# Kernel tuning notes

Hardware: AMD Instinct MI355X
Metric: run time of the kernel (lower is better)

Reference implementation:

```python
import jax, jax.numpy as jnp
import numpy as np

B, T, CIN = 8, 1024, 6
D, L = 128, 2
DI, DS, DC, DTR = 256, 32, 4, 8  # d_inner=expand*d_model, d_state, d_conv, dt_rank=ceil(D/16)
BN_EPS = 1e-5


def setup_inputs() -> dict:
    key = jax.random.key(0)
    ks = jax.random.split(key, 8)
    s = 0.02
    A_log = jnp.log(jnp.broadcast_to(jnp.arange(1, DS + 1, dtype=jnp.float32), (L, DI, DS)))  # S4D-real init
    return {
        "x": jax.random.normal(ks[0], (B, T, CIN), jnp.float32),
        "conv_fw": jax.random.normal(ks[1], (D, CIN, 3), jnp.float32) * s,
        "conv_fb": jnp.zeros((D,), jnp.float32),
        "bn_g": jnp.ones((D,), jnp.float32),
        "bn_b": jnp.zeros((D,), jnp.float32),
        "rms_w": jnp.ones((L, D), jnp.float32),
        "W_in": jax.random.normal(ks[2], (L, D, 2 * DI), jnp.float32) * s,
        "conv_w": jax.random.normal(ks[3], (L, DI, DC), jnp.float32) * s,
        "conv_b": jnp.zeros((L, DI), jnp.float32),
        "W_xproj": jax.random.normal(ks[4], (L, DI, DTR + 2 * DS), jnp.float32) * s,
        "W_dt": jax.random.normal(ks[5], (L, DTR, DI), jnp.float32) * s,
        "b_dt": jnp.zeros((L, DI), jnp.float32),
        "A_log": A_log,
        "D_param": jnp.ones((L, DI), jnp.float32),
        "W_out": jax.random.normal(ks[6], (L, DI, D), jnp.float32) * s,
        "alpha": jnp.full((L,), 0.6, jnp.float32),
        "beta": jnp.full((L,), 0.99, jnp.float32),
        "norm_w": jnp.ones((D,), jnp.float32),
    }


def rmsnorm(x, w, eps=1e-6):
    return x * w * jax.lax.rsqrt(jnp.mean(x * x, axis=-1, keepdims=True) + eps)


def _mamba_block(x, rms_w, W_in, conv_w, conv_b, W_xproj, W_dt, b_dt, A_log, D_param, W_out, a, b):
    # pre-norm residual momentum-Mamba block; x: (B,T,D)
    xz = rmsnorm(x, rms_w) @ W_in            # (B,T,2*DI)
    xc, z = jnp.split(xz, 2, axis=-1)
    # depthwise causal conv over time
    xc = jnp.transpose(xc, (0, 2, 1))        # (B,DI,T)
    xc = jax.lax.conv_general_dilated(xc, conv_w[:, None, :], (1,), [(DC - 1, 0)],
                                      dimension_numbers=("NCH", "OIH", "NCH"), feature_group_count=DI)
    xc = jax.nn.silu(xc + conv_b[None, :, None])
    xc = jnp.transpose(xc, (0, 2, 1))        # (B,T,DI)
    xdbl = xc @ W_xproj                      # (B,T,DTR+2*DS)
    dtl, Bm, Cm = jnp.split(xdbl, [DTR, DTR + DS], axis=-1)
    dt = jax.nn.softplus(dtl @ W_dt + b_dt)  # (B,T,DI)
    A = -jnp.exp(A_log)                      # (DI,DS)
    dA = jnp.exp(dt[..., None] * A)          # (B,T,DI,DS)
    dBx = (dt * xc)[..., None] * Bm[:, :, None, :]  # (B,T,DI,DS)

    def step(carry, inp):
        h, v = carry
        dA_t, dBx_t, C_t = inp
        v = b * v + dBx_t                    # momentum accumulator (mode='real')
        h = dA_t * h + (1.0 - a) * dBx_t + a * v
        y = jnp.einsum("bds,bs->bd", h, C_t)
        return (h, v), y

    h0 = jnp.zeros((x.shape[0], DI, DS), x.dtype)
    _, ys = jax.lax.scan(step, (h0, h0),
                         (jnp.swapaxes(dA, 0, 1), jnp.swapaxes(dBx, 0, 1), jnp.swapaxes(Cm, 0, 1)))
    y = jnp.swapaxes(ys, 0, 1) + D_param * xc
    y = y * jax.nn.silu(z)
    return x + y @ W_out


def reference(x, conv_fw, conv_fb, bn_g, bn_b, rms_w, W_in, conv_w, conv_b, W_xproj,
              W_dt, b_dt, A_log, D_param, W_out, alpha, beta, norm_w):
    # frontend: Conv1d(k=3,pad=1) + BatchNorm1d(eval, running mean 0 var 1) + ReLU (dropout=identity in eval)
    h = jax.lax.conv_general_dilated(jnp.transpose(x, (0, 2, 1)), conv_fw, (1,), [(1, 1)],
                                     dimension_numbers=("NCH", "OIH", "NCH"))
    h = h + conv_fb[None, :, None]
    h = h * (bn_g / jnp.sqrt(1.0 + BN_EPS))[None, :, None] + bn_b[None, :, None]
    h = jax.nn.relu(h)
    h = jnp.transpose(h, (0, 2, 1))          # (B,T,D)
    for i in range(L):
        h = _mamba_block(h, rms_w[i], W_in[i], conv_w[i], conv_b[i], W_xproj[i], W_dt[i],
                         b_dt[i], A_log[i], D_param[i], W_out[i], alpha[i], beta[i])
    return rmsnorm(h, norm_w)
```

## Files before the change

kernel.cpp:

```cpp
#include <hip/hip_runtime.h>
#include <hip/hip_bf16.h>
#include <math.h>

constexpr int Bb  = 8;
constexpr int Tt  = 1024;
constexpr int CIN = 6;
constexpr int Dd  = 128;
constexpr int Ll  = 2;
constexpr int DI  = 256;
constexpr int DS  = 32;
constexpr int DC  = 4;
constexpr int DTR = 8;
constexpr int NX  = DTR + 2 * DS;
constexpr int NXP = 128;
constexpr int ROWS = Bb * Tt;

using u16 = unsigned short;
using u32 = unsigned int;

typedef __attribute__((ext_vector_type(8))) short short8b;
typedef __attribute__((ext_vector_type(4))) float f32x4;

__device__ __forceinline__ float f4c(const float4& v, int k) {
  return k == 0 ? v.x : k == 1 ? v.y : k == 2 ? v.z : v.w;
}

__device__ __forceinline__ u16 f2bf(float f) {
  u32 x = __float_as_uint(f);
  u32 r = (x + 0x7fffu + ((x >> 16) & 1u)) >> 16;
  return (u16)r;
}
__device__ __forceinline__ u32 pack2bf(float lo, float hi) {
  return (u32)f2bf(lo) | ((u32)f2bf(hi) << 16);
}

template <int CTRL, int ROW_MASK>
__device__ __forceinline__ float dpp_add(float x) {
  int m = __builtin_amdgcn_update_dpp(0, __float_as_int(x), CTRL, ROW_MASK, 0xF, true);
  return x + __int_as_float(m);
}
__device__ __forceinline__ float half_wave_sum31(float p) {
  p = dpp_add<0x111, 0xF>(p);
  p = dpp_add<0x112, 0xF>(p);
  p = dpp_add<0x114, 0xF>(p);
  p = dpp_add<0x118, 0xF>(p);
  p = dpp_add<0x142, 0xA>(p);
  return p;
}

__global__ __launch_bounds__(128) void frontend_k(
    const float* __restrict__ x, const float* __restrict__ fw,
    const float* __restrict__ fb, const float* __restrict__ g,
    const float* __restrict__ bnb, float* __restrict__ h) {
  int t = blockIdx.x, b = blockIdx.y, d = threadIdx.x;
  float acc = 0.f;
#pragma unroll
  for (int k = 0; k < 3; ++k) {
    int tt = t - 1 + k;
    if (tt < 0 || tt >= Tt) continue;
    const float* xp = x + ((size_t)b * Tt + tt) * CIN;
#pragma unroll
    for (int c = 0; c < CIN; ++c)
      acc = fmaf(xp[c], fw[(d * CIN + c) * 3 + k], acc);
  }
  float scale = g[d] * rsqrtf(1.f + 1e-5f);
  float val = scale * (acc + fb[d]) + bnb[d];
  h[((size_t)b * Tt + t) * Dd + d] = fmaxf(val, 0.f);
}

__global__ __launch_bounds__(256) void rms_k(const float* __restrict__ in,
                                             const float* __restrict__ w,
                                             float* __restrict__ out) {
  int lane = threadIdx.x & 63;
  int row  = blockIdx.x * 4 + (threadIdx.x >> 6);
  const float* p = in + (size_t)row * Dd;
  float x0 = p[lane], x1 = p[lane + 64];
  float ss = fmaf(x0, x0, x1 * x1);
#pragma unroll
  for (int m = 1; m < 64; m <<= 1) ss += __shfl_xor(ss, m);
  float rs = rsqrtf(ss * (1.f / Dd) + 1e-6f);
  out[(size_t)row * Dd + lane]      = x0 * w[lane] * rs;
  out[(size_t)row * Dd + lane + 64] = x1 * w[lane + 64] * rs;
}

__global__ __launch_bounds__(256) void wtrans_k(const float* __restrict__ W,
                                                u16* __restrict__ Wt,
                                                int K, int N) {
  __shared__ float tile[32][33];
  int k0 = blockIdx.x * 32, n0 = blockIdx.y * 32;
  size_t lofs = (size_t)blockIdx.z * K * N;
  const float* Wp = W + lofs;
  u16* Wtp = Wt + lofs;
  int j = threadIdx.x & 31, i0 = threadIdx.x >> 5;
#pragma unroll
  for (int ii = 0; ii < 4; ++ii) {
    int k = i0 + ii * 8;
    tile[k][j] = Wp[(size_t)(k0 + k) * N + n0 + j];
  }
  __syncthreads();
  int kp = (threadIdx.x & 15) * 2;
  int nb = threadIdx.x >> 4;
#pragma unroll
  for (int half = 0; half < 2; ++half) {
    int n = nb + half * 16;
    u32 u = (u32)f2bf(tile[kp][n]) | ((u32)f2bf(tile[kp + 1][n]) << 16);
    *(u32*)&Wtp[(size_t)(n0 + n) * K + k0 + kp] = u;
  }
}

__global__ __launch_bounds__(256) void wtransxp_k(const float* __restrict__ W,
                                                  u16* __restrict__ Wt) {
  __shared__ float tile[32][33];
  int k0 = blockIdx.x * 32, n0 = blockIdx.y * 32;
  const float* Wp = W + (size_t)blockIdx.z * DI * NX;
  u16* Wtp = Wt + (size_t)blockIdx.z * NXP * DI;
  int j = threadIdx.x & 31, i0 = threadIdx.x >> 5;
#pragma unroll
  for (int ii = 0; ii < 4; ++ii) {
    int k = i0 + ii * 8;
    int n = n0 + j;
    tile[k][j] = (n < NX) ? Wp[(size_t)(k0 + k) * NX + n] : 0.f;
  }
  __syncthreads();
  int kp = (threadIdx.x & 15) * 2;
  int nb = threadIdx.x >> 4;
#pragma unroll
  for (int half = 0; half < 2; ++half) {
    int n = nb + half * 16;
    u32 u = (u32)f2bf(tile[kp][n]) | ((u32)f2bf(tile[kp + 1][n]) << 16);
    *(u32*)&Wtp[(size_t)(n0 + n) * DI + k0 + kp] = u;
  }
}

__global__ __launch_bounds__(256) void bgemm_rms_k(
    const float* __restrict__ A, const float* __restrict__ w,
    const u16* __restrict__ Wt, float* __restrict__ C, int M, int N) {
  constexpr int BM = 128, BN = 64, K = 128;
  constexpr int LDT = K + 8;
  __shared__ u16 Al[BM][LDT];
  __shared__ u16 Wl[BN][LDT];
  int tid = threadIdx.x;
  int wid = tid >> 6, lane = tid & 63;
  int lrow = lane & 15, kh = lane >> 4;
  int bm = blockIdx.x * BM, bn = blockIdx.y * BN;

  {
    int r = tid >> 1, hf = tid & 1;
    const float* ap = A + (size_t)(bm + r) * K + hf * 64;
    float ss = 0.f;
#pragma unroll
    for (int q = 0; q < 16; ++q) {
      float4 v = *(const float4*)(ap + q * 4);
      ss += v.x * v.x + v.y * v.y + v.z * v.z + v.w * v.w;
    }
    ss += __shfl_xor(ss, 1);
    float rs = rsqrtf(ss * (1.f / Dd) + 1e-6f);
    const float* wp = w + hf * 64;
#pragma unroll
    for (int q = 0; q < 8; ++q) {
      float4 v0 = *(const float4*)(ap + q * 8);
      float4 v1 = *(const float4*)(ap + q * 8 + 4);
      float4 w0 = *(const float4*)(wp + q * 8);
      float4 w1 = *(const float4*)(wp + q * 8 + 4);
      uint4 u;
      u.x = pack2bf(v0.x * w0.x * rs, v0.y * w0.y * rs);
      u.y = pack2bf(v0.z * w0.z * rs, v0.w * w0.w * rs);
      u.z = pack2bf(v1.x * w1.x * rs, v1.y * w1.y * rs);
      u.w = pack2bf(v1.z * w1.z * rs, v1.w * w1.w * rs);
      *(uint4*)&Al[r][hf * 64 + q * 8] = u;
    }
  }
  {
    int n = tid >> 2, q = tid & 3;
    const uint4* wp = (const uint4*)(Wt + (size_t)(bn + n) * K + q * 32);
#pragma unroll
    for (int i = 0; i < 4; ++i)
      *(uint4*)&Wl[n][q * 32 + i * 8] = wp[i];
  }
  __syncthreads();

  f32x4 acc[2][4];
#pragma unroll
  for (int i = 0; i < 2; ++i)
#pragma unroll
    for (int j = 0; j < 4; ++j) acc[i][j] = (f32x4){0.f, 0.f, 0.f, 0.f};

#pragma unroll
  for (int ks = 0; ks < 4; ++ks) {
    short8b afr[2], wfr[4];
#pragma unroll
    for (int i = 0; i < 2; ++i)
      afr[i] = *(const short8b*)&Al[wid * 32 + i * 16 + lrow][ks * 32 + kh * 8];
#pragma unroll
    for (int j = 0; j < 4; ++j)
      wfr[j] = *(const short8b*)&Wl[j * 16 + lrow][ks * 32 + kh * 8];
#pragma unroll
    for (int i = 0; i < 2; ++i)
#pragma unroll
      for (int j = 0; j < 4; ++j)
        acc[i][j] = __builtin_amdgcn_mfma_f32_16x16x32_bf16(
            afr[i], wfr[j], acc[i][j], 0, 0, 0);
  }

#pragma unroll
  for (int i = 0; i < 2; ++i)
#pragma unroll
    for (int j = 0; j < 4; ++j)
#pragma unroll
      for (int rg = 0; rg < 4; ++rg) {
        int row = bm + wid * 32 + i * 16 + kh * 4 + rg;
        int col = bn + j * 16 + lrow;
        C[(size_t)row * N + col] = acc[i][j][rg];
      }
}

template <bool ADD_C>
__global__ __launch_bounds__(256) void bgemm_k(
    const float* __restrict__ A, const u16* __restrict__ Wt,
    float* __restrict__ C, int M, int N, int K) {
  constexpr int BM = 128, BN = 64, BK = 32;
  constexpr int LDT = BK + 8;
  __shared__ u16 Al[BM][LDT];
  __shared__ u16 Wl[BN][LDT];
  int tid = threadIdx.x;
  int wid = tid >> 6, lane = tid & 63;
  int lrow = lane & 15, kh = lane >> 4;
  int bm = blockIdx.x * BM, bn = blockIdx.y * BN;

  f32x4 acc[2][4];
#pragma unroll
  for (int i = 0; i < 2; ++i)
#pragma unroll
    for (int j = 0; j < 4; ++j) acc[i][j] = (f32x4){0.f, 0.f, 0.f, 0.f};

  for (int k0 = 0; k0 < K; k0 += BK) {
    {
      int r = tid >> 1, hf = tid & 1;
      const float* ap = A + (size_t)(bm + r) * K + k0 + hf * 16;
      float4 a0 = *(const float4*)(ap + 0);
      float4 a1 = *(const float4*)(ap + 4);
      float4 a2 = *(const float4*)(ap + 8);
      float4 a3 = *(const float4*)(ap + 12);
      uint4 w0, w1;
      w0.x = pack2bf(a0.x, a0.y); w0.y = pack2bf(a0.z, a0.w);
      w0.z = pack2bf(a1.x, a1.y); w0.w = pack2bf(a1.z, a1.w);
      w1.x = pack2bf(a2.x, a2.y); w1.y = pack2bf(a2.z, a2.w);
      w1.z = pack2bf(a3.x, a3.y); w1.w = pack2bf(a3.z, a3.w);
      *(uint4*)&Al[r][hf * 16]     = w0;
      *(uint4*)&Al[r][hf * 16 + 8] = w1;
    }
    if (tid < 128) {
      int n = tid >> 1, hf = tid & 1;
      const uint4* wp = (const uint4*)(Wt + (size_t)(bn + n) * K + k0 + hf * 16);
      uint4 v0 = wp[0], v1 = wp[1];
      *(uint4*)&Wl[n][hf * 16]     = v0;
      *(uint4*)&Wl[n][hf * 16 + 8] = v1;
    }
    __syncthreads();

    short8b afr[2], wfr[4];
#pragma unroll
    for (int i = 0; i < 2; ++i)
      afr[i] = *(const short8b*)&Al[wid * 32 + i * 16 + lrow][kh * 8];
#pragma unroll
    for (int j = 0; j < 4; ++j)
      wfr[j] = *(const short8b*)&Wl[j * 16 + lrow][kh * 8];
#pragma unroll
    for (int i = 0; i < 2; ++i)
#pragma unroll
      for (int j = 0; j < 4; ++j)
        acc[i][j] = __builtin_amdgcn_mfma_f32_16x16x32_bf16(
            afr[i], wfr[j], acc[i][j], 0, 0, 0);
    __syncthreads();
  }

#pragma unroll
  for (int i = 0; i < 2; ++i)
#pragma unroll
    for (int j = 0; j < 4; ++j)
#pragma unroll
      for (int rg = 0; rg < 4; ++rg) {
        int row = bm + wid * 32 + i * 16 + kh * 4 + rg;
        int col = bn + j * 16 + lrow;
        size_t off = (size_t)row * N + col;
        C[off] = acc[i][j][rg] + (ADD_C ? C[off] : 0.f);
      }
}

__global__ __launch_bounds__(256) void bgemm_xp_k(
    const float* __restrict__ A, const u16* __restrict__ Wt,
    float* __restrict__ C) {
  constexpr int BM = 128, BN = 64, BK = 32, K = DI;
  constexpr int LDT = BK + 8;
  __shared__ u16 Al[BM][LDT];
  __shared__ u16 Wl[BN][LDT];
  int tid = threadIdx.x;
  int wid = tid >> 6, lane = tid & 63;
  int lrow = lane & 15, kh = lane >> 4;
  int bm = blockIdx.x * BM, bn = blockIdx.y * BN;

  f32x4 acc[2][4];
#pragma unroll
  for (int i = 0; i < 2; ++i)
#pragma unroll
    for (int j = 0; j < 4; ++j) acc[i][j] = (f32x4){0.f, 0.f, 0.f, 0.f};

  for (int k0 = 0; k0 < K; k0 += BK) {
    {
      int r = tid >> 1, hf = tid & 1;
      const float* ap = A + (size_t)(bm + r) * K + k0 + hf * 16;
      float4 a0 = *(const float4*)(ap + 0);
      float4 a1 = *(const float4*)(ap + 4);
      float4 a2 = *(const float4*)(ap + 8);
      float4 a3 = *(const float4*)(ap + 12);
      uint4 w0, w1;
      w0.x = pack2bf(a0.x, a0.y); w0.y = pack2bf(a0.z, a0.w);
      w0.z = pack2bf(a1.x, a1.y); w0.w = pack2bf(a1.z, a1.w);
      w1.x = pack2bf(a2.x, a2.y); w1.y = pack2bf(a2.z, a2.w);
      w1.z = pack2bf(a3.x, a3.y); w1.w = pack2bf(a3.z, a3.w);
      *(uint4*)&Al[r][hf * 16]     = w0;
      *(uint4*)&Al[r][hf * 16 + 8] = w1;
    }
    if (tid < 128) {
      int n = tid >> 1, hf = tid & 1;
      const uint4* wp = (const uint4*)(Wt + (size_t)(bn + n) * K + k0 + hf * 16);
      uint4 v0 = wp[0], v1 = wp[1];
      *(uint4*)&Wl[n][hf * 16]     = v0;
      *(uint4*)&Wl[n][hf * 16 + 8] = v1;
    }
    __syncthreads();

    short8b afr[2], wfr[4];
#pragma unroll
    for (int i = 0; i < 2; ++i)
      afr[i] = *(const short8b*)&Al[wid * 32 + i * 16 + lrow][kh * 8];
#pragma unroll
    for (int j = 0; j < 4; ++j)
      wfr[j] = *(const short8b*)&Wl[j * 16 + lrow][kh * 8];
#pragma unroll
    for (int i = 0; i < 2; ++i)
#pragma unroll
      for (int j = 0; j < 4; ++j)
        acc[i][j] = __builtin_amdgcn_mfma_f32_16x16x32_bf16(
            afr[i], wfr[j], acc[i][j], 0, 0, 0);
    __syncthreads();
  }

#pragma unroll
  for (int i = 0; i < 2; ++i)
#pragma unroll
    for (int j = 0; j < 4; ++j)
#pragma unroll
      for (int rg = 0; rg < 4; ++rg) {
        int row = bm + wid * 32 + i * 16 + kh * 4 + rg;
        int col = bn + j * 16 + lrow;
        if (col < NX) C[(size_t)row * NX + col] = acc[i][j][rg];
      }
}

__global__ __launch_bounds__(256) void convdw4_k(const float* __restrict__ xz,
                                                 const float* __restrict__ cw,
                                                 const float* __restrict__ cb,
                                                 float* __restrict__ xc) {
  int idx = blockIdx.x * 256 + threadIdx.x;
  int di4 = (idx & 63) * 4;
  int bt  = idx >> 6;
  int t   = bt & (Tt - 1);
  float4 w0 = *(const float4*)&cw[(di4 + 0) * DC];
  float4 w1 = *(const float4*)&cw[(di4 + 1) * DC];
  float4 w2 = *(const float4*)&cw[(di4 + 2) * DC];
  float4 w3 = *(const float4*)&cw[(di4 + 3) * DC];
  float4 a = *(const float4*)&cb[di4];
#pragma unroll
  for (int k = 0; k < DC; ++k) {
    int tt = t - (DC - 1) + k;
    if (tt >= 0) {
      float4 v = *(const float4*)&xz[(size_t)(bt - t + tt) * (2 * DI) + di4];
      a.x = fmaf(v.x, f4c(w0, k), a.x);
      a.y = fmaf(v.y, f4c(w1, k), a.y);
      a.z = fmaf(v.z, f4c(w2, k), a.z);
      a.w = fmaf(v.w, f4c(w3, k), a.w);
    }
  }
  float4 o;
  o.x = a.x / (1.f + expf(-a.x));
  o.y = a.y / (1.f + expf(-a.y));
  o.z = a.z / (1.f + expf(-a.z));
  o.w = a.w / (1.f + expf(-a.w));
  *(float4*)&xc[(size_t)bt * DI + di4] = o;
}

__global__ __launch_bounds__(256) void trans_k(
    const float* __restrict__ xdbl, const float* __restrict__ xc,
    const float* __restrict__ Wdt, const float* __restrict__ bdt,
    float* __restrict__ dtT, float* __restrict__ uT, float* __restrict__ bcT) {
  __shared__ float t1[32][33];
  __shared__ float t2[32][33];
  __shared__ float dtl[32][9];
  __shared__ float wts[8][33];
  __shared__ float bts[32];
  int t0 = blockIdx.x * 32, b = blockIdx.z, y = blockIdx.y;
  int tid = threadIdx.x;
  int j = tid & 31, i0 = tid >> 5;
  if (y < 8) {
    int di0 = y * 32;
    {
      int r = tid >> 3, c = tid & 7;
      dtl[r][c] = xdbl[((size_t)b * Tt + t0 + r) * NX + c];
      wts[i0][j] = Wdt[i0 * DI + di0 + j];
      if (tid < 32) bts[tid] = bdt[di0 + tid];
    }
    __syncthreads();
#pragma unroll
    for (int ii = 0; ii < 4; ++ii) {
      int i = i0 + ii * 8;
      float sacc = bts[j];
#pragma unroll
      for (int r = 0; r < 8; ++r) sacc = fmaf(dtl[i][r], wts[r][j], sacc);
      float sp = fmaxf(sacc, 0.f) + log1pf(expf(-fabsf(sacc)));
      float xcv = xc[((size_t)b * Tt + t0 + i) * DI + di0 + j];
      t1[i][j] = sp;
      t2[i][j] = sp * xcv;
    }
    __syncthreads();
#pragma unroll
    for (int ii = 0; ii < 4; ++ii) {
      int i = i0 + ii * 8;
      dtT[((size_t)b * DI + di0 + i) * Tt + t0 + j] = t1[j][i];
      uT [((size_t)b * DI + di0 + i) * Tt + t0 + j] = t2[j][i];
    }
  } else {
    int k0 = (y - 8) * 32;
#pragma unroll
    for (int ii = 0; ii < 4; ++ii) {
      int i = i0 + ii * 8;
      t1[i][j] = xdbl[((size_t)b * Tt + t0 + i) * NX + 8 + k0 + j];
    }
    __syncthreads();
#pragma unroll
    for (int ii = 0; ii < 4; ++ii) {
      int i = i0 + ii * 8;
      bcT[((size_t)b * 64 + k0 + i) * Tt + t0 + j] = t1[j][i];
    }
  }
}

__global__ __launch_bounds__(256) void scan2_k(
    const float* __restrict__ dtT, const float* __restrict__ uT,
    const float* __restrict__ bcT, const float* __restrict__ A_log,
    const float* __restrict__ alpha, const float* __restrict__ beta,
    float* __restrict__ pT, int layer) {
  int b = blockIdx.y;
  int hw = threadIdx.x >> 5, s = threadIdx.x & 31;
  int di = blockIdx.x * 8 + hw;
  float a = alpha[layer], bc = beta[layer], ab = a * bc;
  float Al2 = -expf(A_log[di * DS + s]) * 1.4426950408889634f;
  const float* dp = dtT + ((size_t)b * DI + di) * Tt;
  const float* up = uT  + ((size_t)b * DI + di) * Tt;
  const float* Bp = bcT + ((size_t)b * 64 + s) * Tt;
  const float* Cp = bcT + ((size_t)b * 64 + 32 + s) * Tt;
  float* pp = pT + ((size_t)b * DI + di) * Tt;

  float h = 0.f, v = 0.f;
  float4 dA_[4], uA_[4], BA_[4], CA_[4];
  float4 dB_[4], uB_[4], BB_[4], CB_[4];

  auto LOAD = [&](float4* d4, float4* u4, float4* B4, float4* C4, int c) {
    int t0 = c * 16;
#pragma unroll
    for (int q = 0; q < 4; ++q) {
      d4[q] = *(const float4*)(dp + t0 + q * 4);
      u4[q] = *(const float4*)(up + t0 + q * 4);
      B4[q] = *(const float4*)(Bp + t0 + q * 4);
      C4[q] = *(const float4*)(Cp + t0 + q * 4);
    }
  };
  auto COMP = [&](const float4* d4, const float4* u4, const float4* B4,
                  const float4* C4, int c) {
    int t0 = c * 16;
    float4 pv;
#pragma unroll
    for (int kk = 0; kk < 16; ++kk) {
      float dA  = exp2f(f4c(d4[kk >> 2], kk & 3) * Al2);
      float dBx = f4c(u4[kk >> 2], kk & 3) * f4c(B4[kk >> 2], kk & 3);
      float u2  = fmaf(ab, v, dBx);
      h = fmaf(dA, h, u2);
      v = fmaf(bc, v, dBx);
      float p = half_wave_sum31(h * f4c(C4[kk >> 2], kk & 3));
      if ((kk & 3) == 0) pv.x = p;
      else if ((kk & 3) == 1) pv.y = p;
      else if ((kk & 3) == 2) pv.z = p;
      else {
        pv.w = p;
        if (s == 31) *(float4*)(pp + t0 + (kk - 3)) = pv;
      }
    }
  };

  constexpr int NC = Tt / 16;
  LOAD(dA_, uA_, BA_, CA_, 0);
  for (int c = 0; c < NC; c += 2) {
    LOAD(dB_, uB_, BB_, CB_, c + 1);
    COMP(dA_, uA_, BA_, CA_, c);
    LOAD(dA_, uA_, BA_, CA_, (c + 2 < NC) ? c + 2 : NC - 1);
    COMP(dB_, uB_, BB_, CB_, c + 1);
  }
}

__global__ __launch_bounds__(256) void gate_k(
    const float* __restrict__ pT, const float* __restrict__ xc,
    const float* __restrict__ xz, const float* __restrict__ Dp_,
    float* __restrict__ y) {
  __shared__ float tile[32][33];
  int t0 = blockIdx.x * 32, di0 = blockIdx.y * 32, b = blockIdx.z;
  int j = threadIdx.x & 31, i0 = threadIdx.x >> 5;
#pragma unroll
  for (int ii = 0; ii < 4; ++ii) {
    int r = i0 + ii * 8;
    tile[r][j] = pT[((size_t)b * DI + di0 + r) * Tt + t0 + j];
  }
  __syncthreads();
#pragma unroll
  for (int ii = 0; ii < 4; ++ii) {
    int i = i0 + ii * 8;
    size_t row = (size_t)b * Tt + t0 + i;
    float p   = tile[j][i];
    float xcv = xc[row * DI + di0 + j];
    float zz  = xz[row * (2 * DI) + DI + di0 + j];
    float g   = zz / (1.f + expf(-zz));
    y[row * DI + di0 + j] = fmaf(Dp_[di0 + j], xcv, p) * g;
  }
}

extern "C" void kernel_launch(void* const* d_in, const int* in_sizes, int n_in,
                              void* d_out, int out_size, void* d_ws, size_t ws_size,
                              hipStream_t stream) {
  const float* x       = (const float*)d_in[0];
  const float* conv_fw = (const float*)d_in[1];
  const float* conv_fb = (const float*)d_in[2];
  const float* bn_g    = (const float*)d_in[3];
  const float* bn_b    = (const float*)d_in[4];
  const float* rms_w   = (const float*)d_in[5];
  const float* W_in    = (const float*)d_in[6];
  const float* conv_w  = (const float*)d_in[7];
  const float* conv_b  = (const float*)d_in[8];
  const float* W_xp    = (const float*)d_in[9];
  const float* W_dt    = (const float*)d_in[10];
  const float* b_dt    = (const float*)d_in[11];
  const float* A_log   = (const float*)d_in[12];
  const float* D_par   = (const float*)d_in[13];
  const float* W_out   = (const float*)d_in[14];
  const float* alpha   = (const float*)d_in[15];
  const float* beta    = (const float*)d_in[16];
  const float* norm_w  = (const float*)d_in[17];
  float* out = (float*)d_out;

  float* ws   = (float*)d_ws;
  float* h    = ws;
  float* xz   = h + 1048576;
  float* xc   = xz + 4194304;
  float* xdbl = xc + 2097152;
  float* pT   = xdbl + 589824;
  float* uT   = pT + 2097152;
  float* bcT  = uT + 2097152;
  float* shrd = bcT + 524288;
  u16*  wt_in  = (u16*)(shrd + 2097152);
  u16*  wt_out = wt_in + 2 * (2 * DI) * Dd;
  u16*  wt_xp  = wt_out + 2 * Dd * DI;
  float* dtT  = shrd;
  float* ytot = shrd;

  wtrans_k<<<dim3(Dd / 32, (2 * DI) / 32, Ll), 256, 0, stream>>>(
      W_in, wt_in, Dd, 2 * DI);
  wtrans_k<<<dim3(DI / 32, Dd / 32, Ll), 256, 0, stream>>>(
      W_out, wt_out, DI, Dd);
  wtransxp_k<<<dim3(DI / 32, NXP / 32, Ll), 256, 0, stream>>>(W_xp, wt_xp);

  frontend_k<<<dim3(Tt, Bb), 128, 0, stream>>>(x, conv_fw, conv_fb, bn_g, bn_b, h);

  for (int l = 0; l < Ll; ++l) {
    bgemm_rms_k<<<dim3(ROWS / 128, (2 * DI) / 64), 256, 0, stream>>>(
        h, rms_w + l * Dd, wt_in + (size_t)l * (2 * DI) * Dd, xz, ROWS, 2 * DI);
    convdw4_k<<<(ROWS * (DI / 4)) / 256, 256, 0, stream>>>(
        xz, conv_w + l * DI * DC, conv_b + l * DI, xc);
    bgemm_xp_k<<<dim3(ROWS / 128, 2), 256, 0, stream>>>(
        xc, wt_xp + (size_t)l * NXP * DI, xdbl);
    trans_k<<<dim3(Tt / 32, 10, Bb), 256, 0, stream>>>(
        xdbl, xc, W_dt + l * DTR * DI, b_dt + l * DI, dtT, uT, bcT);
    scan2_k<<<dim3(DI / 8, Bb), 256, 0, stream>>>(
        dtT, uT, bcT, A_log + l * DI * DS, alpha, beta, pT, l);
    gate_k<<<dim3(Tt / 32, DI / 32, Bb), 256, 0, stream>>>(
        pT, xc, xz, D_par + l * DI, ytot);
    bgemm_k<true><<<dim3(ROWS / 128, Dd / 64), 256, 0, stream>>>(
        ytot, wt_out + (size_t)l * Dd * DI, h, ROWS, Dd, DI);
  }

  rms_k<<<ROWS / 4, 256, 0, stream>>>(h, norm_w, out);
}
```

Before: 403.3 us.

## Fuse gating into output-projection GEMM A-tile load

```diff
diff --git a/kernel.cpp b/kernel.cpp
--- a/kernel.cpp
+++ b/kernel.cpp
@@ -214,11 +214,10 @@
       }
 }
 
-template <bool ADD_C>
-__global__ __launch_bounds__(256) void bgemm_k(
+__global__ __launch_bounds__(256) void bgemm_xp_k(
     const float* __restrict__ A, const u16* __restrict__ Wt,
-    float* __restrict__ C, int M, int N, int K) {
-  constexpr int BM = 128, BN = 64, BK = 32;
+    float* __restrict__ C) {
+  constexpr int BM = 128, BN = 64, BK = 32, K = DI;
   constexpr int LDT = BK + 8;
   __shared__ u16 Al[BM][LDT];
   __shared__ u16 Wl[BN][LDT];
@@ -282,22 +281,24 @@
       for (int rg = 0; rg < 4; ++rg) {
         int row = bm + wid * 32 + i * 16 + kh * 4 + rg;
         int col = bn + j * 16 + lrow;
-        size_t off = (size_t)row * N + col;
-        C[off] = acc[i][j][rg] + (ADD_C ? C[off] : 0.f);
+        if (col < NX) C[(size_t)row * NX + col] = acc[i][j][rg];
       }
 }
 
-__global__ __launch_bounds__(256) void bgemm_xp_k(
-    const float* __restrict__ A, const u16* __restrict__ Wt,
-    float* __restrict__ C) {
-  constexpr int BM = 128, BN = 64, BK = 32, K = DI;
+__global__ __launch_bounds__(256) void bgemm_gate_k(
+    const float* __restrict__ pT, const float* __restrict__ xc,
+    const float* __restrict__ xz, const float* __restrict__ Dp_,
+    const u16* __restrict__ Wt, float* __restrict__ C) {
+  constexpr int BM = 128, BN = 64, BK = 32, K = DI, N = Dd;
   constexpr int LDT = BK + 8;
   __shared__ u16 Al[BM][LDT];
   __shared__ u16 Wl[BN][LDT];
+  __shared__ float pl[BK][BM + 4];
   int tid = threadIdx.x;
   int wid = tid >> 6, lane = tid & 63;
   int lrow = lane & 15, kh = lane >> 4;
   int bm = blockIdx.x * BM, bn = blockIdx.y * BN;
+  int b  = bm / Tt, t0 = bm & (Tt - 1);
 
   f32x4 acc[2][4];
 #pragma unroll
@@ -307,19 +308,16 @@
 
   for (int k0 = 0; k0 < K; k0 += BK) {
     {
-      int r = tid >> 1, hf = tid & 1;
-      const float* ap = A + (size_t)(bm + r) * K + k0 + hf * 16;
-      float4 a0 = *(const float4*)(ap + 0);
-      float4 a1 = *(const float4*)(ap + 4);
-      float4 a2 = *(const float4*)(ap + 8);
-      float4 a3 = *(const float4*)(ap + 12);
-      uint4 w0, w1;
-      w0.x = pack2bf(a0.x, a0.y); w0.y = pack2bf(a0.z, a0.w);
-      w0.z = pack2bf(a1.x, a1.y); w0.w = pack2bf(a1.z, a1.w);
-      w1.x = pack2bf(a2.x, a2.y); w1.y = pack2bf(a2.z, a2.w);
-      w1.z = pack2bf(a3.x, a3.y); w1.w = pack2bf(a3.z, a3.w);
-      *(uint4*)&Al[r][hf * 16]     = w0;
-      *(uint4*)&Al[r][hf * 16 + 8] = w1;
+      int kk = tid >> 3, q = tid & 7;
+      const float* pp = pT + ((size_t)b * DI + k0 + kk) * Tt + t0 + q * 16;
+      float4 v0 = *(const float4*)(pp + 0);
+      float4 v1 = *(const float4*)(pp + 4);
+      float4 v2 = *(const float4*)(pp + 8);
+      float4 v3 = *(const float4*)(pp + 12);
+      *(float4*)&pl[kk][q * 16 + 0]  = v0;
+      *(float4*)&pl[kk][q * 16 + 4]  = v1;
+      *(float4*)&pl[kk][q * 16 + 8]  = v2;
+      *(float4*)&pl[kk][q * 16 + 12] = v3;
     }
     if (tid < 128) {
       int n = tid >> 1, hf = tid & 1;
@@ -329,6 +327,36 @@
       *(uint4*)&Wl[n][hf * 16 + 8] = v1;
     }
     __syncthreads();
+    {
+      int r = tid >> 1, hf = tid & 1;
+      size_t row = (size_t)(bm + r);
+      const float* xcp = xc + row * DI + k0 + hf * 16;
+      const float* zp  = xz + row * (2 * DI) + DI + k0 + hf * 16;
+      const float* dp_ = Dp_ + k0 + hf * 16;
+      float yv[16];
+#pragma unroll
+      for (int q = 0; q < 4; ++q) {
+        float4 xcv = *(const float4*)(xcp + q * 4);
+        float4 zz  = *(const float4*)(zp + q * 4);
+        float4 dd  = *(const float4*)(dp_ + q * 4);
+        int kb = hf * 16 + q * 4;
+        float p0 = pl[kb + 0][r], p1 = pl[kb + 1][r];
+        float p2 = pl[kb + 2][r], p3 = pl[kb + 3][r];
+        yv[q * 4 + 0] = fmaf(dd.x, xcv.x, p0) * (zz.x / (1.f + expf(-zz.x)));
+        yv[q * 4 + 1] = fmaf(dd.y, xcv.y, p1) * (zz.y / (1.f + expf(-zz.y)));
+        yv[q * 4 + 2] = fmaf(dd.z, xcv.z, p2) * (zz.z / (1.f + expf(-zz.z)));
+        yv[q * 4 + 3] = fmaf(dd.w, xcv.w, p3) * (zz.w / (1.f + expf(-zz.w)));
+      }
+      uint4 u0;
+      u0.x = pack2bf(yv[0], yv[1]);  u0.y = pack2bf(yv[2], yv[3]);
+      u0.z = pack2bf(yv[4], yv[5]);  u0.w = pack2bf(yv[6], yv[7]);
+      uint4 u1;
+      u1.x = pack2bf(yv[8], yv[9]);  u1.y = pack2bf(yv[10], yv[11]);
+      u1.z = pack2bf(yv[12], yv[13]); u1.w = pack2bf(yv[14], yv[15]);
+      *(uint4*)&Al[r][hf * 16]     = u0;
+      *(uint4*)&Al[r][hf * 16 + 8] = u1;
+    }
+    __syncthreads();
 
     short8b afr[2], wfr[4];
 #pragma unroll
@@ -354,7 +382,8 @@
       for (int rg = 0; rg < 4; ++rg) {
         int row = bm + wid * 32 + i * 16 + kh * 4 + rg;
         int col = bn + j * 16 + lrow;
-        if (col < NX) C[(size_t)row * NX + col] = acc[i][j][rg];
+        size_t off = (size_t)row * N + col;
+        C[off] = acc[i][j][rg] + C[off];
       }
 }
 
@@ -504,31 +533,6 @@
     COMP(dA_, uA_, BA_, CA_, c);
     LOAD(dA_, uA_, BA_, CA_, (c + 2 < NC) ? c + 2 : NC - 1);
     COMP(dB_, uB_, BB_, CB_, c + 1);
-  }
-}
-
-__global__ __launch_bounds__(256) void gate_k(
-    const float* __restrict__ pT, const float* __restrict__ xc,
-    const float* __restrict__ xz, const float* __restrict__ Dp_,
-    float* __restrict__ y) {
-  __shared__ float tile[32][33];
-  int t0 = blockIdx.x * 32, di0 = blockIdx.y * 32, b = blockIdx.z;
-  int j = threadIdx.x & 31, i0 = threadIdx.x >> 5;
-#pragma unroll
-  for (int ii = 0; ii < 4; ++ii) {
-    int r = i0 + ii * 8;
-    tile[r][j] = pT[((size_t)b * DI + di0 + r) * Tt + t0 + j];
-  }
-  __syncthreads();
-#pragma unroll
-  for (int ii = 0; ii < 4; ++ii) {
-    int i = i0 + ii * 8;
-    size_t row = (size_t)b * Tt + t0 + i;
-    float p   = tile[j][i];
-    float xcv = xc[row * DI + di0 + j];
-    float zz  = xz[row * (2 * DI) + DI + di0 + j];
-    float g   = zz / (1.f + expf(-zz));
-    y[row * DI + di0 + j] = fmaf(Dp_[di0 + j], xcv, p) * g;
   }
 }
 
@@ -563,12 +567,10 @@
   float* pT   = xdbl + 589824;
   float* uT   = pT + 2097152;
   float* bcT  = uT + 2097152;
-  float* shrd = bcT + 524288;
-  u16*  wt_in  = (u16*)(shrd + 2097152);
+  float* dtT  = bcT + 524288;
+  u16*  wt_in  = (u16*)(dtT + 2097152);
   u16*  wt_out = wt_in + 2 * (2 * DI) * Dd;
   u16*  wt_xp  = wt_out + 2 * Dd * DI;
-  float* dtT  = shrd;
-  float* ytot = shrd;
 
   wtrans_k<<<dim3(Dd / 32, (2 * DI) / 32, Ll), 256, 0, stream>>>(
       W_in, wt_in, Dd, 2 * DI);
@@ -589,10 +591,8 @@
         xdbl, xc, W_dt + l * DTR * DI, b_dt + l * DI, dtT, uT, bcT);
     scan2_k<<<dim3(DI / 8, Bb), 256, 0, stream>>>(
         dtT, uT, bcT, A_log + l * DI * DS, alpha, beta, pT, l);
-    gate_k<<<dim3(Tt / 32, DI / 32, Bb), 256, 0, stream>>>(
-        pT, xc, xz, D_par + l * DI, ytot);
-    bgemm_k<true><<<dim3(ROWS / 128, Dd / 64), 256, 0, stream>>>(
-        ytot, wt_out + (size_t)l * Dd * DI, h, ROWS, Dd, DI);
+    bgemm_gate_k<<<dim3(ROWS / 128, Dd / 64), 256, 0, stream>>>(
+        pT, xc, xz, D_par + l * DI, wt_out + (size_t)l * Dd * DI, h);
   }
 
   rms_k<<<ROWS / 4, 256, 0, stream>>>(h, norm_w, out);
```

Result: slower. 411.4 us (+2.0%).
